# Kernel tuning notes

Measured on AMD Instinct MI355X. Metric: run time of the kernel, lower is better.

Reference implementation:

```python
import jax, jax.numpy as jnp
import numpy as np

IN_FEATURE = 256
OUT_FEATURE = 128
ALPHA = 0.5  # LeakyReLU negative slope
NEG_BIG = -9e15


def setup_inputs() -> dict:
    key = jax.random.key(0)
    k1, k2, k3, k4 = jax.random.split(key, 4)
    N = 8192
    x = jax.random.normal(k1, (N, IN_FEATURE), dtype=jnp.float32)
    adj = jax.random.randint(k2, (N, N), 0, 2, dtype=jnp.int32)
    stdv = 1.0 / np.sqrt(OUT_FEATURE)
    W = jax.random.uniform(k3, (IN_FEATURE, OUT_FEATURE), dtype=jnp.float32,
                           minval=-stdv, maxval=stdv)
    a = jax.random.uniform(k4, (2 * OUT_FEATURE, 1), dtype=jnp.float32,
                           minval=-stdv, maxval=stdv)
    return {"input": x, "adj": adj, "W": W, "a": a}


def reference(input, adj, W, a):
    # h: [N, F_out]
    h = input @ W
    # Additive attention: cat([h_i, h_j]) @ a == h_i @ a1 + h_j @ a2
    a1 = a[:OUT_FEATURE, 0]   # [F_out]
    a2 = a[OUT_FEATURE:, 0]   # [F_out]
    f1 = h @ a1               # [N]  (row / source contribution)
    f2 = h @ a2               # [N]  (col / target contribution)
    e = jax.nn.leaky_relu(f1[:, None] + f2[None, :], negative_slope=ALPHA)  # [N, N]
    scores = jnp.where(adj > 0, e, NEG_BIG)
    attention = jax.nn.softmax(scores, axis=1)  # [N, N]
    h_prime = attention @ h                     # [N, F_out]
    return jax.nn.elu(h_prime)
```

## Files before the change

kernel.cpp:

```cpp
#include <hip/hip_runtime.h>

#define N_NODES 8192
#define IN_F 256
#define OUT_F 128
#define ALPHA 0.5f
#define JC 8
#define KCHUNK 1024
#define RK 128
#define ROUNDS 8
#define RSTEPS 4

using short8 = __attribute__((ext_vector_type(8))) short;
using f32x4  = __attribute__((ext_vector_type(4))) float;

__device__ __forceinline__ unsigned int f2bf(float f){
  unsigned int u = __float_as_uint(f);
  u += 0x7fffu + ((u >> 16) & 1u);
  return u >> 16;
}
__device__ __forceinline__ float bf2f(short s){
  return __uint_as_float(((unsigned int)(unsigned short)s) << 16);
}

__global__ __launch_bounds__(256) void k_h(const float* __restrict__ x,
                                           const float* __restrict__ W,
                                           float* __restrict__ h){
  __shared__ float xs[16*IN_F];
  const int tid = threadIdx.x;
  const int r0 = blockIdx.x * 16;
  const float4* xg = (const float4*)(x + (size_t)r0*IN_F);
  float4* xl = (float4*)xs;
  #pragma unroll
  for(int i=0;i<4;i++) xl[tid + i*256] = xg[tid + i*256];
  __syncthreads();
  const int wave = tid >> 6, lane = tid & 63;
  float2 acc[4];
  #pragma unroll
  for(int j=0;j<4;j++){ acc[j].x = 0.f; acc[j].y = 0.f; }
  const float2* Wp = (const float2*)W;
  for(int k4=0;k4<IN_F;k4+=4){
    float4 xq[4];
    #pragma unroll
    for(int j=0;j<4;j++) xq[j] = *(const float4*)&xs[(wave*4+j)*IN_F + k4];
    #pragma unroll
    for(int kk=0;kk<4;kk++){
      float2 wv = Wp[(size_t)(k4+kk)*64 + lane];
      #pragma unroll
      for(int j=0;j<4;j++){
        float xv = kk==0?xq[j].x : kk==1?xq[j].y : kk==2?xq[j].z : xq[j].w;
        acc[j].x += xv*wv.x; acc[j].y += xv*wv.y;
      }
    }
  }
  #pragma unroll
  for(int j=0;j<4;j++)
    *(float2*)(h + (size_t)(r0 + wave*4 + j)*OUT_F + lane*2) = acc[j];
}

__global__ __launch_bounds__(256) void k_f(const float* __restrict__ h,
                                           const float* __restrict__ a,
                                           float* __restrict__ f1,
                                           float* __restrict__ f2){
  const int wave = threadIdx.x >> 6, lane = threadIdx.x & 63;
  const int row = blockIdx.x*4 + wave;
  float2 hv = ((const float2*)(h + (size_t)row*OUT_F))[lane];
  float2 a1 = ((const float2*)a)[lane];
  float2 a2 = ((const float2*)(a + OUT_F))[lane];
  float s1 = hv.x*a1.x + hv.y*a1.y;
  float s2 = hv.x*a2.x + hv.y*a2.y;
  #pragma unroll
  for(int off=32; off; off>>=1){
    s1 += __shfl_down(s1, off);
    s2 += __shfl_down(s2, off);
  }
  if(lane == 0){ f1[row] = s1; f2[row] = s2; }
}

#define LDW 132
__global__ __launch_bounds__(256) void k_pack(const float* __restrict__ h,
                                              unsigned short* __restrict__ P){
  __shared__ float ld[32*LDW];
  const int tid = threadIdx.x;
  const int kb = blockIdx.x, j0 = kb*32;
  #pragma unroll
  for(int i=0;i<4;i++){
    int idx = tid + i*256;
    int row = idx >> 5, c4 = (idx & 31)*4;
    *(float4*)&ld[row*LDW + c4] = *(const float4*)(h + (size_t)(j0+row)*OUT_F + c4);
  }
  __syncthreads();
  #pragma unroll
  for(int i=0;i<2;i++){
    int o = tid*2 + i;
    int c = o >> 6, lane = o & 63;
    int q = lane >> 4, n = lane & 15;
    short8 v;
    #pragma unroll
    for(int t=0;t<8;t++) v[t] = (short)f2bf(ld[(q*8+t)*LDW + c*16 + n]);
    *(short8*)(P + ((size_t)(kb*8 + c)*64 + lane)*8) = v;
  }
}

__global__ __launch_bounds__(256, 2) void k_attn(const int* __restrict__ adj,
    const unsigned short* __restrict__ P,
    const float* __restrict__ f1, const float* __restrict__ f2,
    float* __restrict__ part, float* __restrict__ denp){
  __shared__ __align__(16) unsigned short Alds[128*RK];
  __shared__ __align__(16) short Blds[RK*OUT_F];
  __shared__ float f1s[128];
  const int tid = threadIdx.x;
  const int wave = tid >> 6, lane = tid & 63;
  const int m = lane & 15, q = lane >> 4;
  const int jc = blockIdx.x;
  const int r0b = blockIdx.y * 128;
  const int jb = jc * KCHUNK;
  const int kb0 = jc * (KCHUNK/32);
  const int srow = tid >> 5;
  const int sc0  = (tid & 31) * 4;
  const int swz  = ((((sc0 >> 3) ^ srow) << 4) | ((sc0 & 4) << 1));

  if(tid < 128) f1s[tid] = f1[r0b + tid];

  f32x4 acc0[8], acc1[8];
  #pragma unroll
  for(int c=0;c<8;c++){ acc0[c] = (f32x4){0,0,0,0}; acc1[c] = (f32x4){0,0,0,0}; }
  float den0 = 0.f, den1 = 0.f;

  const char* Ab = (const char*)Alds;
  char* Aw = (char*)Alds + swz;
  const int mw = m & 7;
  const int rg0 = wave*32 + m;

  __syncthreads();

  for(int rd=0; rd<ROUNDS; rd++){
    const int kbase = jb + rd*RK;
    const int4* Pb = (const int4*)(P + ((size_t)(kb0 + rd*4) << 12));
    int4* Bl4 = (int4*)Blds;
    #pragma unroll
    for(int i=0;i<8;i++) Bl4[i*256 + tid] = Pb[i*256 + tid];
    float4 fv = *(const float4*)(f2 + kbase + sc0);
    const char* ap = (const char*)adj + (((size_t)(r0b + srow)*N_NODES + kbase + sc0) << 2);
    #pragma unroll 4
    for(int i=0;i<16;i++){
      int4 av = *(const int4*)(ap + ((size_t)i*8*N_NODES << 2));
      float f1v = f1s[i*8 + srow];
      float t0 = f1v + fv.x, t1 = f1v + fv.y, t2 = f1v + fv.z, t3 = f1v + fv.w;
      t0 = t0 > 0.f ? t0 : ALPHA*t0;  t1 = t1 > 0.f ? t1 : ALPHA*t1;
      t2 = t2 > 0.f ? t2 : ALPHA*t2;  t3 = t3 > 0.f ? t3 : ALPHA*t3;
      float w0 = av.x > 0 ? __expf(t0) : 0.f;
      float w1 = av.y > 0 ? __expf(t1) : 0.f;
      float w2 = av.z > 0 ? __expf(t2) : 0.f;
      float w3 = av.w > 0 ? __expf(t3) : 0.f;
      uint2 pk;
      pk.x = f2bf(w0) | (f2bf(w1) << 16);
      pk.y = f2bf(w2) | (f2bf(w3) << 16);
      *(uint2*)(Aw + (i*8 + srow)*(RK*2)) = pk;
    }
    __syncthreads();
    #pragma unroll
    for(int s=0;s<RSTEPS;s++){
      const int gq = ((s*4 + q) ^ mw) << 4;
      short8 A0 = *(const short8*)(Ab + rg0*(RK*2) + gq);
      short8 A1 = *(const short8*)(Ab + (rg0+16)*(RK*2) + gq);
      #pragma unroll
      for(int t=0;t<8;t++){ den0 += bf2f(A0[t]); den1 += bf2f(A1[t]); }
      const short8* Bl = (const short8*)Blds + s*512 + lane;
      #pragma unroll
      for(int c=0;c<8;c++){
        short8 Bf = Bl[c*64];
        acc0[c] = __builtin_amdgcn_mfma_f32_16x16x32_bf16(A0, Bf, acc0[c], 0,0,0);
        acc1[c] = __builtin_amdgcn_mfma_f32_16x16x32_bf16(A1, Bf, acc1[c], 0,0,0);
      }
    }
    __syncthreads();
  }

  den0 += __shfl_down(den0, 32); den0 += __shfl_down(den0, 16);
  den1 += __shfl_down(den1, 32); den1 += __shfl_down(den1, 16);
  const int r0w = r0b + wave*32;
  if(lane < 16){
    denp[(size_t)jc*N_NODES + r0w + lane]      = den0;
    denp[(size_t)jc*N_NODES + r0w + 16 + lane] = den1;
  }
  float* pp = part + (size_t)jc*N_NODES*OUT_F;
  #pragma unroll
  for(int c=0;c<8;c++){
    #pragma unroll
    for(int reg=0;reg<4;reg++){
      pp[(size_t)(r0w + q*4 + reg)*OUT_F      + c*16 + m] = acc0[c][reg];
      pp[(size_t)(r0w + 16 + q*4 + reg)*OUT_F + c*16 + m] = acc1[c][reg];
    }
  }
}

__global__ __launch_bounds__(256) void k_out(const float* __restrict__ part,
    const float* __restrict__ denp, float* __restrict__ out){
  const int idx = blockIdx.x*256 + threadIdx.x;
  const int r = idx >> 7;
  float v = 0.f, d = 0.f;
  #pragma unroll
  for(int p=0;p<JC;p++){
    v += part[(size_t)p*N_NODES*OUT_F + idx];
    d += denp[(size_t)p*N_NODES + r];
  }
  v /= d;
  out[idx] = v > 0.f ? v : (__expf(v) - 1.f);
}

extern "C" void kernel_launch(void* const* d_in, const int* in_sizes, int n_in,
                              void* d_out, int out_size, void* d_ws, size_t ws_size,
                              hipStream_t stream){
  const float* x   = (const float*)d_in[0];
  const int*   adj = (const int*)d_in[1];
  const float* W   = (const float*)d_in[2];
  const float* a   = (const float*)d_in[3];
  char* ws = (char*)d_ws;
  float* h            = (float*)ws;
  unsigned short* P   = (unsigned short*)(ws + (4u<<20));
  float* f1           = (float*)(ws + (6u<<20));
  float* f2           = (float*)(ws + (6u<<20) + (32u<<10));
  float* part         = (float*)(ws + (8u<<20));
  float* denp         = (float*)(ws + (40u<<20));
  float* out          = (float*)d_out;

  k_h<<<512, 256, 0, stream>>>(x, W, h);
  k_f<<<2048, 256, 0, stream>>>(h, a, f1, f2);
  k_pack<<<256, 256, 0, stream>>>(h, P);
  k_attn<<<dim3(JC,64), 256, 0, stream>>>(adj, P, f1, f2, part, denp);
  k_out<<<(N_NODES*OUT_F)/256, 256, 0, stream>>>(part, denp, out);
}
```

Baseline: 411.2 us.

## Fuse h/f/pack kernels, prefetch adj into registers, retile attention blocks

Merges the projection, attention-logit and bf16 packing kernels into one kernel, so h never goes to global memory and two launches disappear. The attention kernel now works on 64-row blocks with one MFMA accumulator set per wave and longer 2048-column chunks (4 splits instead of 8). The next round's adj tile and f2 slice are loaded into registers while the current round's weights are computed. This cuts partial-sum traffic and hides adj load latency, at the cost of reloading each B tile for half as many rows.

```diff
diff --git a/kernel.cpp b/kernel.cpp
--- a/kernel.cpp
+++ b/kernel.cpp
@@ -4,10 +4,10 @@
 #define IN_F 256
 #define OUT_F 128
 #define ALPHA 0.5f
-#define JC 8
-#define KCHUNK 1024
+#define JC 4
+#define KCHUNK 2048
 #define RK 128
-#define ROUNDS 8
+#define ROUNDS 16
 #define RSTEPS 4
 
 using short8 = __attribute__((ext_vector_type(8))) short;
@@ -22,12 +22,16 @@
   return __uint_as_float(((unsigned int)(unsigned short)s) << 16);
 }
 
-__global__ __launch_bounds__(256) void k_h(const float* __restrict__ x,
-                                           const float* __restrict__ W,
-                                           float* __restrict__ h){
+__global__ __launch_bounds__(256) void k_hfp(const float* __restrict__ x,
+                                             const float* __restrict__ W,
+                                             const float* __restrict__ a,
+                                             unsigned short* __restrict__ P,
+                                             float* __restrict__ f1,
+                                             float* __restrict__ f2){
   __shared__ float xs[16*IN_F];
   const int tid = threadIdx.x;
-  const int r0 = blockIdx.x * 16;
+  const int bx = blockIdx.x;
+  const int r0 = bx * 16;
   const float4* xg = (const float4*)(x + (size_t)r0*IN_F);
   float4* xl = (float4*)xs;
   #pragma unroll
@@ -52,98 +56,78 @@
       }
     }
   }
-  #pragma unroll
-  for(int j=0;j<4;j++)
-    *(float2*)(h + (size_t)(r0 + wave*4 + j)*OUT_F + lane*2) = acc[j];
-}
-
-__global__ __launch_bounds__(256) void k_f(const float* __restrict__ h,
-                                           const float* __restrict__ a,
-                                           float* __restrict__ f1,
-                                           float* __restrict__ f2){
-  const int wave = threadIdx.x >> 6, lane = threadIdx.x & 63;
-  const int row = blockIdx.x*4 + wave;
-  float2 hv = ((const float2*)(h + (size_t)row*OUT_F))[lane];
-  float2 a1 = ((const float2*)a)[lane];
-  float2 a2 = ((const float2*)(a + OUT_F))[lane];
-  float s1 = hv.x*a1.x + hv.y*a1.y;
-  float s2 = hv.x*a2.x + hv.y*a2.y;
-  #pragma unroll
-  for(int off=32; off; off>>=1){
-    s1 += __shfl_down(s1, off);
-    s2 += __shfl_down(s2, off);
-  }
-  if(lane == 0){ f1[row] = s1; f2[row] = s2; }
-}
-
-#define LDW 132
-__global__ __launch_bounds__(256) void k_pack(const float* __restrict__ h,
-                                              unsigned short* __restrict__ P){
-  __shared__ float ld[32*LDW];
-  const int tid = threadIdx.x;
-  const int kb = blockIdx.x, j0 = kb*32;
-  #pragma unroll
-  for(int i=0;i<4;i++){
-    int idx = tid + i*256;
-    int row = idx >> 5, c4 = (idx & 31)*4;
-    *(float4*)&ld[row*LDW + c4] = *(const float4*)(h + (size_t)(j0+row)*OUT_F + c4);
-  }
-  __syncthreads();
-  #pragma unroll
-  for(int i=0;i<2;i++){
-    int o = tid*2 + i;
-    int c = o >> 6, lane = o & 63;
-    int q = lane >> 4, n = lane & 15;
-    short8 v;
-    #pragma unroll
-    for(int t=0;t<8;t++) v[t] = (short)f2bf(ld[(q*8+t)*LDW + c*16 + n]);
-    *(short8*)(P + ((size_t)(kb*8 + c)*64 + lane)*8) = v;
-  }
+  float2 av1 = ((const float2*)a)[lane];
+  float2 av2 = ((const float2*)(a + OUT_F))[lane];
+  #pragma unroll
+  for(int j=0;j<4;j++){
+    float s1 = acc[j].x*av1.x + acc[j].y*av1.y;
+    float s2 = acc[j].x*av2.x + acc[j].y*av2.y;
+    #pragma unroll
+    for(int off=32; off; off>>=1){
+      s1 += __shfl_down(s1, off);
+      s2 += __shfl_down(s2, off);
+    }
+    if(lane == 0){ f1[r0 + wave*4 + j] = s1; f2[r0 + wave*4 + j] = s2; }
+  }
+  __syncthreads();
+  #pragma unroll
+  for(int j=0;j<4;j++) *(float2*)&xs[(wave*4+j)*132 + lane*2] = acc[j];
+  __syncthreads();
+  const int kb = bx >> 1, half = bx & 1;
+  const int c = tid >> 5, ql = (tid >> 4) & 1, n = tid & 15;
+  short8 v;
+  #pragma unroll
+  for(int t=0;t<8;t++) v[t] = (short)f2bf(xs[(ql*8+t)*132 + c*16 + n]);
+  *(short8*)(P + ((size_t)((kb*8 + c)*64 + half*32 + ql*16 + n))*8) = v;
 }
 
 __global__ __launch_bounds__(256, 2) void k_attn(const int* __restrict__ adj,
     const unsigned short* __restrict__ P,
     const float* __restrict__ f1, const float* __restrict__ f2,
     float* __restrict__ part, float* __restrict__ denp){
-  __shared__ __align__(16) unsigned short Alds[128*RK];
+  __shared__ __align__(16) unsigned short Alds[64*RK];
   __shared__ __align__(16) short Blds[RK*OUT_F];
-  __shared__ float f1s[128];
+  __shared__ float f1s[64];
   const int tid = threadIdx.x;
   const int wave = tid >> 6, lane = tid & 63;
   const int m = lane & 15, q = lane >> 4;
   const int jc = blockIdx.x;
-  const int r0b = blockIdx.y * 128;
+  const int r0b = blockIdx.y * 64;
   const int jb = jc * KCHUNK;
   const int kb0 = jc * (KCHUNK/32);
   const int srow = tid >> 5;
   const int sc0  = (tid & 31) * 4;
   const int swz  = ((((sc0 >> 3) ^ srow) << 4) | ((sc0 & 4) << 1));
 
-  if(tid < 128) f1s[tid] = f1[r0b + tid];
-
-  f32x4 acc0[8], acc1[8];
-  #pragma unroll
-  for(int c=0;c<8;c++){ acc0[c] = (f32x4){0,0,0,0}; acc1[c] = (f32x4){0,0,0,0}; }
-  float den0 = 0.f, den1 = 0.f;
+  if(tid < 64) f1s[tid] = f1[r0b + tid];
+
+  f32x4 acc0[8];
+  #pragma unroll
+  for(int c=0;c<8;c++) acc0[c] = (f32x4){0,0,0,0};
+  float den0 = 0.f;
 
   const char* Ab = (const char*)Alds;
   char* Aw = (char*)Alds + swz;
   const int mw = m & 7;
-  const int rg0 = wave*32 + m;
+  const int rg0 = wave*16 + m;
+
+  const size_t rowstride = (size_t)N_NODES * 4;
+  const char* ap0 = (const char*)adj + (((size_t)(r0b + srow)*N_NODES + jb + sc0) << 2);
+  int4 adjv[8];
+  #pragma unroll
+  for(int i=0;i<8;i++) adjv[i] = *(const int4*)(ap0 + (size_t)i*8*rowstride);
+  float4 fv = *(const float4*)(f2 + jb + sc0);
 
   __syncthreads();
 
   for(int rd=0; rd<ROUNDS; rd++){
-    const int kbase = jb + rd*RK;
     const int4* Pb = (const int4*)(P + ((size_t)(kb0 + rd*4) << 12));
     int4* Bl4 = (int4*)Blds;
     #pragma unroll
     for(int i=0;i<8;i++) Bl4[i*256 + tid] = Pb[i*256 + tid];
-    float4 fv = *(const float4*)(f2 + kbase + sc0);
-    const char* ap = (const char*)adj + (((size_t)(r0b + srow)*N_NODES + kbase + sc0) << 2);
-    #pragma unroll 4
-    for(int i=0;i<16;i++){
-      int4 av = *(const int4*)(ap + ((size_t)i*8*N_NODES << 2));
+    #pragma unroll
+    for(int i=0;i<8;i++){
+      int4 av = adjv[i];
       float f1v = f1s[i*8 + srow];
       float t0 = f1v + fv.x, t1 = f1v + fv.y, t2 = f1v + fv.z, t3 = f1v + fv.w;
       t0 = t0 > 0.f ? t0 : ALPHA*t0;  t1 = t1 > 0.f ? t1 : ALPHA*t1;
@@ -157,40 +141,37 @@
       pk.y = f2bf(w2) | (f2bf(w3) << 16);
       *(uint2*)(Aw + (i*8 + srow)*(RK*2)) = pk;
     }
+    const int rdn = (rd+1 < ROUNDS) ? rd+1 : rd;
+    const char* apn = ap0 + (size_t)(rdn*RK) * 4;
+    #pragma unroll
+    for(int i=0;i<8;i++) adjv[i] = *(const int4*)(apn + (size_t)i*8*rowstride);
+    fv = *(const float4*)(f2 + jb + rdn*RK + sc0);
     __syncthreads();
     #pragma unroll
     for(int s=0;s<RSTEPS;s++){
       const int gq = ((s*4 + q) ^ mw) << 4;
       short8 A0 = *(const short8*)(Ab + rg0*(RK*2) + gq);
-      short8 A1 = *(const short8*)(Ab + (rg0+16)*(RK*2) + gq);
       #pragma unroll
-      for(int t=0;t<8;t++){ den0 += bf2f(A0[t]); den1 += bf2f(A1[t]); }
+      for(int t=0;t<8;t++) den0 += bf2f(A0[t]);
       const short8* Bl = (const short8*)Blds + s*512 + lane;
       #pragma unroll
       for(int c=0;c<8;c++){
         short8 Bf = Bl[c*64];
         acc0[c] = __builtin_amdgcn_mfma_f32_16x16x32_bf16(A0, Bf, acc0[c], 0,0,0);
-        acc1[c] = __builtin_amdgcn_mfma_f32_16x16x32_bf16(A1, Bf, acc1[c], 0,0,0);
       }
     }
     __syncthreads();
   }
 
   den0 += __shfl_down(den0, 32); den0 += __shfl_down(den0, 16);
-  den1 += __shfl_down(den1, 32); den1 += __shfl_down(den1, 16);
-  const int r0w = r0b + wave*32;
-  if(lane < 16){
-    denp[(size_t)jc*N_NODES + r0w + lane]      = den0;
-    denp[(size_t)jc*N_NODES + r0w + 16 + lane] = den1;
-  }
+  const int r0w = r0b + wave*16;
+  if(lane < 16) denp[(size_t)jc*N_NODES + r0w + lane] = den0;
   float* pp = part + (size_t)jc*N_NODES*OUT_F;
   #pragma unroll
   for(int c=0;c<8;c++){
     #pragma unroll
-    for(int reg=0;reg<4;reg++){
-      pp[(size_t)(r0w + q*4 + reg)*OUT_F      + c*16 + m] = acc0[c][reg];
-      pp[(size_t)(r0w + 16 + q*4 + reg)*OUT_F + c*16 + m] = acc1[c][reg];
-    }
+    for(int reg=0;reg<4;reg++)
+      pp[(size_t)(r0w + q*4 + reg)*OUT_F + c*16 + m] = acc0[c][reg];
   }
 }
 
@@ -216,17 +197,14 @@
   const float* W   = (const float*)d_in[2];
   const float* a   = (const float*)d_in[3];
   char* ws = (char*)d_ws;
-  float* h            = (float*)ws;
-  unsigned short* P   = (unsigned short*)(ws + (4u<<20));
-  float* f1           = (float*)(ws + (6u<<20));
-  float* f2           = (float*)(ws + (6u<<20) + (32u<<10));
-  float* part         = (float*)(ws + (8u<<20));
-  float* denp         = (float*)(ws + (40u<<20));
-  float* out          = (float*)d_out;
-
-  k_h<<<512, 256, 0, stream>>>(x, W, h);
-  k_f<<<2048, 256, 0, stream>>>(h, a, f1, f2);
-  k_pack<<<256, 256, 0, stream>>>(h, P);
-  k_attn<<<dim3(JC,64), 256, 0, stream>>>(adj, P, f1, f2, part, denp);
+  unsigned short* P = (unsigned short*)ws;
+  float* f1         = (float*)(ws + (2u<<20));
+  float* f2         = (float*)(ws + (2u<<20) + (32u<<10));
+  float* part       = (float*)(ws + (4u<<20));
+  float* denp       = (float*)(ws + (20u<<20));
+  float* out        = (float*)d_out;
+
+  k_hfp<<<512, 256, 0, stream>>>(x, W, a, P, f1, f2);
+  k_attn<<<dim3(JC,128), 256, 0, stream>>>(adj, P, f1, f2, part, denp);
   k_out<<<(N_NODES*OUT_F)/256, 256, 0, stream>>>(part, denp, out);
 }
```

Result: slower. 428.4 us (+4.2%).
